# Kernel optimization log

Measured on AMD Instinct MI355X. Metric: run time of the kernel, lower is better.

## Reference

```python
import jax, jax.numpy as jnp
import numpy as np

N = 50000       # nodes
E_RAND = 800000 # random edges (avg degree ~16)
K = 64          # edges touching `node`; setup_inputs guarantees exactly K
F = 64          # num_node_features
C = 64          # conv_channels


def setup_inputs() -> dict:
    key = jax.random.key(0)
    ks = jax.random.split(key, 6)
    x = jax.random.normal(ks[0], (N, F), dtype=jnp.float32)
    # random edges avoiding node 0 so exactly the K prepended edges touch node 0
    src = jax.random.randint(ks[1], (E_RAND,), 1, N, dtype=jnp.int64)
    dst = jax.random.randint(ks[2], (E_RAND,), 1, N, dtype=jnp.int64)
    ksrc = jnp.zeros((K,), dtype=jnp.int64)
    kdst = jnp.arange(1, K + 1, dtype=jnp.int64)
    edge_index = jnp.stack([jnp.concatenate([ksrc, src]),
                            jnp.concatenate([kdst, dst])])  # [2, K+E_RAND]
    W1 = jax.random.normal(ks[3], (F, C), jnp.float32) / np.float32(np.sqrt(F))
    b1 = jnp.zeros((C,), jnp.float32)
    W2 = jax.random.normal(ks[4], (C, C), jnp.float32) / np.float32(np.sqrt(C))
    b2 = jnp.zeros((C,), jnp.float32)
    Wr = jax.random.normal(ks[5], (C, 1), jnp.float32) / np.float32(np.sqrt(C))
    br = jnp.zeros((1,), jnp.float32)
    return {"x": x, "edge_index": edge_index, "node": 0,
            "W1": W1, "b1": b1, "W2": W2, "b2": b2, "Wr": Wr, "br": br}


def gcn_conv(x, src, dst, W, b):
    """PyG GCNConv with self-loops already appended to (src, dst).
    out[v] = sum_{(u,v)} deg(u)^-1/2 * deg(v)^-1/2 * (x @ W)[u] + b
    """
    n = x.shape[0]
    xw = x @ W                                              # [N, C]
    deg = jnp.zeros((n,), xw.dtype).at[dst].add(1.0)        # in-degree incl. self-loop
    dinv = jnp.where(deg > 0, jax.lax.rsqrt(deg), 0.0)
    norm = dinv[src] * dinv[dst]                            # [E]
    out = jax.ops.segment_sum(xw[src] * norm[:, None], dst, num_segments=n)
    return out + b


def reference(x, edge_index, node, W1, b1, W2, b2, Wr, br):
    n = x.shape[0]
    loop = jnp.arange(n, dtype=edge_index.dtype)
    src = jnp.concatenate([edge_index[0], loop])  # add self loops (GCNConv default)
    dst = jnp.concatenate([edge_index[1], loop])
    h = jax.nn.relu(gcn_conv(x, src, dst, W1, b1))
    h = jax.nn.relu(gcn_conv(h, src, dst, W2, b2))
    # edges incident to `node` (setup guarantees exactly K such edges)
    s0, d0 = edge_index[0], edge_index[1]
    mask = (s0 == node) | (d0 == node)
    idx = jnp.nonzero(mask, size=K)[0]
    s, d = s0[idx], d0[idx]
    targets = jnp.where(s == node, d, s)  # self-loop (s==d==node) -> node
    score = h[targets] @ Wr + br          # [K, 1]
    score = jax.nn.softmax(score, axis=0)
    return score[:, 0], targets
```

## Files before the change

kernel.cpp:

```cpp
#include <hip/hip_runtime.h>
#include <math.h>

#define KK 64
#define CAP 64
#define NF 4160
#define BMW 1568

__global__ __launch_bounds__(256) void k_find(const int* __restrict__ ei, int E,
                                              const int* __restrict__ nodep,
                                              int4* __restrict__ zbase, int zcount4,
                                              int* __restrict__ tcount,
                                              int* __restrict__ tpairs,
                                              float* __restrict__ h1s) {
    int idx = blockIdx.x * 256 + threadIdx.x;
    if (idx < zcount4) zbase[idx] = make_int4(0, 0, 0, 0);
    if (idx < 64) h1s[(size_t)NF * 64 + idx] = 0.f;
    int node = nodep[0];
    int n4 = E >> 2;
    if (idx < n4) {
        int4 ss = ((const int4*)ei)[idx];
        int4 dd = ((const int4*)(ei + E))[idx];
        int s[4] = {ss.x, ss.y, ss.z, ss.w};
        int d[4] = {dd.x, dd.y, dd.z, dd.w};
#pragma unroll
        for (int k = 0; k < 4; k++) {
            if (s[k] == node || d[k] == node) {
                int q = atomicAdd(tcount, 1);
                if (q < KK) { int e = idx * 4 + k; tpairs[2 * q] = e; tpairs[2 * q + 1] = (s[k] == node) ? d[k] : s[k]; }
            }
        }
    }
    if (idx == 0) {
        for (int e = n4 * 4; e < E; e++) {
            int s = ei[e], d = ei[E + e];
            if (s == node || d == node) {
                int q = atomicAdd(tcount, 1);
                if (q < KK) { tpairs[2 * q] = e; tpairs[2 * q + 1] = (s == node) ? d : s; }
            }
        }
    }
}

__global__ __launch_bounds__(256) void k_collect_t(const int* __restrict__ ei, int E,
                                                   const int* __restrict__ tpairs,
                                                   int* __restrict__ cnt,
                                                   int* __restrict__ tcnt2,
                                                   int* __restrict__ tslots,
                                                   int* __restrict__ tsorted_g,
                                                   int* __restrict__ towner_g) {
    __shared__ unsigned int bmask[BMW];
    __shared__ int tnode[KK];
    __shared__ int eidx[KK], tgt[KK], srt[KK];
    int tid = threadIdx.x;
    for (int i = tid; i < BMW; i += 256) bmask[i] = 0u;
    if (tid < KK) { eidx[tid] = tpairs[2 * tid]; tgt[tid] = tpairs[2 * tid + 1]; }
    __syncthreads();
    if (tid < KK) {
        int rank = 0;
        for (int j = 0; j < KK; j++) rank += (eidx[j] < eidx[tid]) ? 1 : 0;
        srt[rank] = tgt[tid];
    }
    __syncthreads();
    if (tid < KK) {
        int mynode = srt[tid];
        int owner = tid;
        for (int j = 0; j < tid; j++) if (srt[j] == mynode) { owner = j; break; }
        tnode[tid] = (owner == tid) ? mynode : -1;
        if (owner == tid) atomicOr(&bmask[mynode >> 5], 1u << (mynode & 31));
        if (blockIdx.x == 0) { tsorted_g[tid] = mynode; towner_g[tid] = owner; }
    }
    __syncthreads();
    int n4 = E >> 2;
    for (int idx = blockIdx.x * 256 + tid; idx < n4; idx += gridDim.x * 256) {
        int4 ss = ((const int4*)ei)[idx];
        int4 dd = ((const int4*)(ei + E))[idx];
        int s[4] = {ss.x, ss.y, ss.z, ss.w};
        int d[4] = {dd.x, dd.y, dd.z, dd.w};
        atomicAdd(&cnt[d[0]], 1);
        atomicAdd(&cnt[d[1]], 1);
#pragma unroll
        for (int k = 0; k < 4; k++) {
            if ((bmask[d[k] >> 5] >> (d[k] & 31)) & 1u) {
                int f = 0;
                for (int j = 0; j < KK; j++) if (tnode[j] == d[k]) { f = j + 1; break; }
                if (f) { int p = atomicAdd(&tcnt2[f - 1], 1); if (p < CAP) tslots[(f - 1) * CAP + p] = s[k]; }
            }
        }
    }
    if (blockIdx.x == 0 && tid == 0) {
        for (int e = n4 * 4; e < E; e++) {
            int d = ei[E + e];
            atomicAdd(&cnt[d], 1);
            if ((bmask[d >> 5] >> (d & 31)) & 1u) {
                int f = 0;
                for (int j = 0; j < KK; j++) if (tnode[j] == d) { f = j + 1; break; }
                if (f) { int p = atomicAdd(&tcnt2[f - 1], 1); if (p < CAP) tslots[(f - 1) * CAP + p] = ei[e]; }
            }
        }
    }
}

__device__ __forceinline__ int fnode_of(int i, const int* tsorted, const int* towner,
                                        const int* tcnt2, const int* tslots) {
    int tp = i / 65, j = i % 65;
    if (j == 0) return tsorted[tp];
    int own = towner[tp];
    int c = tcnt2[own]; if (c > CAP) c = CAP;
    return (j - 1 < c) ? tslots[own * CAP + (j - 1)] : -1;
}

__global__ __launch_bounds__(1024) void k_fbuild(const int* __restrict__ tsorted,
                                                 const int* __restrict__ towner,
                                                 const int* __restrict__ tcnt2,
                                                 const int* __restrict__ tslots,
                                                 int* __restrict__ fnode,
                                                 int* __restrict__ fmapRow,
                                                 int* __restrict__ fidx,
                                                 unsigned char* __restrict__ fown) {
    int tid = threadIdx.x;
    for (int i = tid; i < NF; i += 1024)
        fnode[i] = fnode_of(i, tsorted, towner, tcnt2, tslots);
    __syncthreads();
    for (int i = tid; i < NF; i += 1024) {
        int u = fnode[i];
        if (u >= 0) atomicCAS(&fmapRow[u], 0, i + 1);
    }
    __syncthreads();
    for (int i = tid; i < NF; i += 1024) {
        int u = fnode[i];
        if (u >= 0) {
            int row = fmapRow[u];
            fidx[i] = row - 1;
            fown[i] = (unsigned char)(row == i + 1);
        } else {
            fidx[i] = NF;
            fown[i] = 0;
        }
    }
}

__global__ __launch_bounds__(256) void k_collect_f(const int* __restrict__ ei, int E,
                                                   const int* __restrict__ fmapRow,
                                                   int* __restrict__ cnt,
                                                   int* __restrict__ fcnt,
                                                   int* __restrict__ fslots) {
    int idx = blockIdx.x * 256 + threadIdx.x;
    int n4 = E >> 2;
    if (idx < n4) {
        int4 ss = ((const int4*)ei)[idx];
        int4 dd = ((const int4*)(ei + E))[idx];
        int s[4] = {ss.x, ss.y, ss.z, ss.w};
        int d[4] = {dd.x, dd.y, dd.z, dd.w};
        atomicAdd(&cnt[d[2]], 1);
        atomicAdd(&cnt[d[3]], 1);
        int r0 = fmapRow[d[0]], r1 = fmapRow[d[1]], r2 = fmapRow[d[2]], r3 = fmapRow[d[3]];
        if (r0) { int p = atomicAdd(&fcnt[r0 - 1], 1); if (p < CAP) fslots[(size_t)(r0 - 1) * CAP + p] = s[0]; }
        if (r1) { int p = atomicAdd(&fcnt[r1 - 1], 1); if (p < CAP) fslots[(size_t)(r1 - 1) * CAP + p] = s[1]; }
        if (r2) { int p = atomicAdd(&fcnt[r2 - 1], 1); if (p < CAP) fslots[(size_t)(r2 - 1) * CAP + p] = s[2]; }
        if (r3) { int p = atomicAdd(&fcnt[r3 - 1], 1); if (p < CAP) fslots[(size_t)(r3 - 1) * CAP + p] = s[3]; }
    }
    if (idx == 0) {
        for (int e = n4 * 4; e < E; e++) {
            int d = ei[E + e];
            atomicAdd(&cnt[d], 1);
            int r = fmapRow[d];
            if (r) { int p = atomicAdd(&fcnt[r - 1], 1); if (p < CAP) fslots[(size_t)(r - 1) * CAP + p] = ei[e]; }
        }
    }
}

__global__ __launch_bounds__(256) void k_layer1(const float* __restrict__ x,
                                                const int* __restrict__ fnode,
                                                const unsigned char* __restrict__ fown,
                                                const int* __restrict__ cnt,
                                                const int* __restrict__ fcnt,
                                                const int* __restrict__ fslots,
                                                const float* __restrict__ W1,
                                                const float* __restrict__ b1,
                                                float* __restrict__ h1s) {
    __shared__ __align__(16) float W1s[64 * 64];
    __shared__ int anyown;
    int tid = threadIdx.x;
    int i = blockIdx.x * 4 + (tid >> 6);
    int lane = tid & 63;
    int own = (i < NF) ? (int)fown[i] : 0;
    if (tid == 0) anyown = 0;
    __syncthreads();
    if (lane == 0 && own) anyown = 1;
    __syncthreads();
    if (!anyown) return;
    for (int j = tid; j < 1024; j += 256) ((float4*)W1s)[j] = ((const float4*)W1)[j];
    __syncthreads();
    if (!own) return;
    int u = fnode[i];
    float du = rsqrtf((float)(cnt[u] + 1));
    float acc = du * x[(size_t)u * 64 + lane];
    int c = fcnt[i]; if (c > CAP) c = CAP;
    const int* sl = fslots + (size_t)i * CAP;
    int k = 0;
    for (; k + 4 <= c; k += 4) {
        int u0 = sl[k], u1 = sl[k + 1], u2 = sl[k + 2], u3 = sl[k + 3];
        float f0 = rsqrtf((float)(cnt[u0] + 1));
        float f1 = rsqrtf((float)(cnt[u1] + 1));
        float f2 = rsqrtf((float)(cnt[u2] + 1));
        float f3 = rsqrtf((float)(cnt[u3] + 1));
        acc += f0 * x[(size_t)u0 * 64 + lane] + f1 * x[(size_t)u1 * 64 + lane]
             + f2 * x[(size_t)u2 * 64 + lane] + f3 * x[(size_t)u3 * 64 + lane];
    }
    for (; k < c; k++) {
        int uu = sl[k];
        acc += rsqrtf((float)(cnt[uu] + 1)) * x[(size_t)uu * 64 + lane];
    }
    float z = du * acc;
    float h = 0.f;
#pragma unroll
    for (int f = 0; f < 64; f++) h += __shfl(z, f) * W1s[f * 64 + lane];
    h = fmaxf(h + b1[lane], 0.f);
    h1s[(size_t)i * 64 + lane] = du * h;
}

__global__ __launch_bounds__(64) void k_score2(const float* __restrict__ h1s,
                                               const int* __restrict__ fidx,
                                               const int* __restrict__ tsorted,
                                               const int* __restrict__ towner,
                                               const int* __restrict__ tcnt2,
                                               const int* __restrict__ cnt,
                                               const float* __restrict__ W2,
                                               const float* __restrict__ b2,
                                               const float* __restrict__ Wr,
                                               float* __restrict__ sc) {
    int tp = blockIdx.x;
    int lane = threadIdx.x;
    int t = tsorted[tp];
    float dt = rsqrtf((float)(cnt[t] + 1));
    int c = tcnt2[towner[tp]]; if (c > CAP) c = CAP;
    int jmax = 1 + c;
    const int* fx = fidx + tp * 65;
    float z = 0.f;
#pragma unroll 8
    for (int j = 0; j < jmax; j++) {
        int idx = fx[j];
        z += h1s[(size_t)idx * 64 + lane];
    }
    z *= dt;
    float acc = 0.f;
#pragma unroll
    for (int f = 0; f < 64; f++) acc += __shfl(z, f) * W2[f * 64 + lane];
    float h2 = fmaxf(acc + b2[lane], 0.f);
    float p = h2 * Wr[lane];
#pragma unroll
    for (int off = 32; off >= 1; off >>= 1) p += __shfl_xor(p, off);
    if (lane == 0) sc[tp] = p;
}

__global__ void k_softmax(const float* __restrict__ sc, const int* __restrict__ tsorted,
                          float* __restrict__ out) {
    int t = threadIdx.x;
    float s = sc[t];
    float m = s;
#pragma unroll
    for (int off = 32; off >= 1; off >>= 1) m = fmaxf(m, __shfl_xor(m, off));
    float e = __expf(s - m);
    float ss = e;
#pragma unroll
    for (int off = 32; off >= 1; off >>= 1) ss += __shfl_xor(ss, off);
    out[t] = e / ss;
    out[KK + t] = (float)tsorted[t];
}

extern "C" void kernel_launch(void* const* d_in, const int* in_sizes, int n_in,
                              void* d_out, int out_size, void* d_ws, size_t ws_size,
                              hipStream_t stream) {
    const float* x  = (const float*)d_in[0];
    const int*   ei = (const int*)d_in[1];
    const int*   nodep = (const int*)d_in[2];
    const float* W1 = (const float*)d_in[3];
    const float* b1 = (const float*)d_in[4];
    const float* W2 = (const float*)d_in[5];
    const float* b2 = (const float*)d_in[6];
    const float* Wr = (const float*)d_in[7];
    const float* br = (const float*)d_in[8];
    float* out = (float*)d_out;
    (void)br;

    int N = in_sizes[0] / 64;
    int E = in_sizes[1] / 2;

    char* w = (char*)d_ws;
    int* cnt     = (int*)w; w += (size_t)N * 4;
    int* fmapRow = (int*)w; w += (size_t)N * 4;
    int* fcnt    = (int*)w; w += (size_t)NF * 4;
    int* tcnt2   = (int*)w; w += KK * 4;
    int zcount4 = (2 * N + NF + KK) / 4;
    int* tcount = (int*)w; w += 16;
    int* tpairs  = (int*)w; w += 2 * KK * 4;
    int* tsorted = (int*)w; w += KK * 4;
    int* towner  = (int*)w; w += KK * 4;
    int* tslots  = (int*)w; w += (size_t)KK * CAP * 4;
    int* fnode   = (int*)w; w += (size_t)NF * 4;
    int* fidx    = (int*)w; w += (size_t)NF * 4;
    unsigned char* fown = (unsigned char*)w; w += (size_t)NF;
    w = (char*)(((size_t)w + 15) & ~(size_t)15);
    int* fslots  = (int*)w; w += (size_t)NF * CAP * 4;
    float* h1s   = (float*)w; w += (size_t)(NF + 1) * 64 * 4;
    float* sc    = (float*)w; w += KK * 4;

    hipMemsetAsync(tcount, 0, 16, stream);

    int n4 = E >> 2;
    int ebl = (n4 + 255) / 256;
    k_find<<<ebl, 256, 0, stream>>>(ei, E, nodep, (int4*)cnt, zcount4, tcount, tpairs, h1s);
    k_collect_t<<<512, 256, 0, stream>>>(ei, E, tpairs, cnt, tcnt2, tslots, tsorted, towner);
    k_fbuild<<<1, 1024, 0, stream>>>(tsorted, towner, tcnt2, tslots, fnode, fmapRow, fidx, fown);
    k_collect_f<<<ebl, 256, 0, stream>>>(ei, E, fmapRow, cnt, fcnt, fslots);
    k_layer1<<<(NF + 3) / 4, 256, 0, stream>>>(x, fnode, fown, cnt, fcnt, fslots, W1, b1, h1s);
    k_score2<<<KK, 64, 0, stream>>>(h1s, fidx, tsorted, towner, tcnt2, cnt, W2, b2, Wr, sc);
    k_softmax<<<1, 64, 0, stream>>>(sc, tsorted, out);
}
```

Measured before the change: 153.2 us.

## Fold feature-row map construction into collect kernel and drop fbuild launch

Removes the single-block k_fbuild kernel. The node-to-row map (fmapRow) is now built with atomicCAS directly inside k_collect_t, as target and neighbor slots are assigned. k_layer1 and k_score2 derive node ids and ownership on the fly from tslots and fmapRow instead of reading precomputed fnode/fidx/fown arrays. This removes a serialized one-block launch and its global round-trips, at the cost of extra atomics in the edge scan and some indirect lookups in the downstream kernels.

```diff
diff --git a/kernel.cpp b/kernel.cpp
--- a/kernel.cpp
+++ b/kernel.cpp
@@ -10,11 +10,9 @@
                                               const int* __restrict__ nodep,
                                               int4* __restrict__ zbase, int zcount4,
                                               int* __restrict__ tcount,
-                                              int* __restrict__ tpairs,
-                                              float* __restrict__ h1s) {
+                                              int* __restrict__ tpairs) {
     int idx = blockIdx.x * 256 + threadIdx.x;
     if (idx < zcount4) zbase[idx] = make_int4(0, 0, 0, 0);
-    if (idx < 64) h1s[(size_t)NF * 64 + idx] = 0.f;
     int node = nodep[0];
     int n4 = E >> 2;
     if (idx < n4) {
@@ -46,6 +44,7 @@
                                                    int* __restrict__ cnt,
                                                    int* __restrict__ tcnt2,
                                                    int* __restrict__ tslots,
+                                                   int* __restrict__ fmapRow,
                                                    int* __restrict__ tsorted_g,
                                                    int* __restrict__ towner_g) {
     __shared__ unsigned int bmask[BMW];
@@ -67,7 +66,10 @@
         for (int j = 0; j < tid; j++) if (srt[j] == mynode) { owner = j; break; }
         tnode[tid] = (owner == tid) ? mynode : -1;
         if (owner == tid) atomicOr(&bmask[mynode >> 5], 1u << (mynode & 31));
-        if (blockIdx.x == 0) { tsorted_g[tid] = mynode; towner_g[tid] = owner; }
+        if (blockIdx.x == 0) {
+            tsorted_g[tid] = mynode; towner_g[tid] = owner;
+            if (owner == tid) atomicCAS(&fmapRow[mynode], 0, tid * 65 + 0 + 1);
+        }
     }
     __syncthreads();
     int n4 = E >> 2;
@@ -83,7 +85,13 @@
             if ((bmask[d[k] >> 5] >> (d[k] & 31)) & 1u) {
                 int f = 0;
                 for (int j = 0; j < KK; j++) if (tnode[j] == d[k]) { f = j + 1; break; }
-                if (f) { int p = atomicAdd(&tcnt2[f - 1], 1); if (p < CAP) tslots[(f - 1) * CAP + p] = s[k]; }
+                if (f) {
+                    int p = atomicAdd(&tcnt2[f - 1], 1);
+                    if (p < CAP) {
+                        tslots[(f - 1) * CAP + p] = s[k];
+                        atomicCAS(&fmapRow[s[k]], 0, (f - 1) * 65 + (p + 1) + 1);
+                    }
+                }
             }
         }
     }
@@ -94,7 +102,13 @@
             if ((bmask[d >> 5] >> (d & 31)) & 1u) {
                 int f = 0;
                 for (int j = 0; j < KK; j++) if (tnode[j] == d) { f = j + 1; break; }
-                if (f) { int p = atomicAdd(&tcnt2[f - 1], 1); if (p < CAP) tslots[(f - 1) * CAP + p] = ei[e]; }
+                if (f) {
+                    int p = atomicAdd(&tcnt2[f - 1], 1);
+                    if (p < CAP) {
+                        tslots[(f - 1) * CAP + p] = ei[e];
+                        atomicCAS(&fmapRow[ei[e]], 0, (f - 1) * 65 + (p + 1) + 1);
+                    }
+                }
             }
         }
     }
@@ -107,36 +121,6 @@
     int own = towner[tp];
     int c = tcnt2[own]; if (c > CAP) c = CAP;
     return (j - 1 < c) ? tslots[own * CAP + (j - 1)] : -1;
-}
-
-__global__ __launch_bounds__(1024) void k_fbuild(const int* __restrict__ tsorted,
-                                                 const int* __restrict__ towner,
-                                                 const int* __restrict__ tcnt2,
-                                                 const int* __restrict__ tslots,
-                                                 int* __restrict__ fnode,
-                                                 int* __restrict__ fmapRow,
-                                                 int* __restrict__ fidx,
-                                                 unsigned char* __restrict__ fown) {
-    int tid = threadIdx.x;
-    for (int i = tid; i < NF; i += 1024)
-        fnode[i] = fnode_of(i, tsorted, towner, tcnt2, tslots);
-    __syncthreads();
-    for (int i = tid; i < NF; i += 1024) {
-        int u = fnode[i];
-        if (u >= 0) atomicCAS(&fmapRow[u], 0, i + 1);
-    }
-    __syncthreads();
-    for (int i = tid; i < NF; i += 1024) {
-        int u = fnode[i];
-        if (u >= 0) {
-            int row = fmapRow[u];
-            fidx[i] = row - 1;
-            fown[i] = (unsigned char)(row == i + 1);
-        } else {
-            fidx[i] = NF;
-            fown[i] = 0;
-        }
-    }
 }
 
 __global__ __launch_bounds__(256) void k_collect_f(const int* __restrict__ ei, int E,
@@ -161,17 +145,18 @@
     }
     if (idx == 0) {
         for (int e = n4 * 4; e < E; e++) {
-            int d = ei[E + e];
-            atomicAdd(&cnt[d], 1);
-            int r = fmapRow[d];
+            int r = fmapRow[ei[E + e]];
             if (r) { int p = atomicAdd(&fcnt[r - 1], 1); if (p < CAP) fslots[(size_t)(r - 1) * CAP + p] = ei[e]; }
         }
     }
 }
 
 __global__ __launch_bounds__(256) void k_layer1(const float* __restrict__ x,
-                                                const int* __restrict__ fnode,
-                                                const unsigned char* __restrict__ fown,
+                                                const int* __restrict__ tsorted,
+                                                const int* __restrict__ towner,
+                                                const int* __restrict__ tcnt2,
+                                                const int* __restrict__ tslots,
+                                                const int* __restrict__ fmapRow,
                                                 const int* __restrict__ cnt,
                                                 const int* __restrict__ fcnt,
                                                 const int* __restrict__ fslots,
@@ -183,7 +168,11 @@
     int tid = threadIdx.x;
     int i = blockIdx.x * 4 + (tid >> 6);
     int lane = tid & 63;
-    int own = (i < NF) ? (int)fown[i] : 0;
+    int u = -1, own = 0;
+    if (i < NF) {
+        u = fnode_of(i, tsorted, towner, tcnt2, tslots);
+        if (u >= 0) own = (fmapRow[u] == i + 1);
+    }
     if (tid == 0) anyown = 0;
     __syncthreads();
     if (lane == 0 && own) anyown = 1;
@@ -192,7 +181,6 @@
     for (int j = tid; j < 1024; j += 256) ((float4*)W1s)[j] = ((const float4*)W1)[j];
     __syncthreads();
     if (!own) return;
-    int u = fnode[i];
     float du = rsqrtf((float)(cnt[u] + 1));
     float acc = du * x[(size_t)u * 64 + lane];
     int c = fcnt[i]; if (c > CAP) c = CAP;
@@ -220,10 +208,11 @@
 }
 
 __global__ __launch_bounds__(64) void k_score2(const float* __restrict__ h1s,
-                                               const int* __restrict__ fidx,
                                                const int* __restrict__ tsorted,
                                                const int* __restrict__ towner,
                                                const int* __restrict__ tcnt2,
+                                               const int* __restrict__ tslots,
+                                               const int* __restrict__ fmapRow,
                                                const int* __restrict__ cnt,
                                                const float* __restrict__ W2,
                                                const float* __restrict__ b2,
@@ -233,14 +222,15 @@
     int lane = threadIdx.x;
     int t = tsorted[tp];
     float dt = rsqrtf((float)(cnt[t] + 1));
-    int c = tcnt2[towner[tp]]; if (c > CAP) c = CAP;
-    int jmax = 1 + c;
-    const int* fx = fidx + tp * 65;
-    float z = 0.f;
+    int own = towner[tp];
+    int c = tcnt2[own]; if (c > CAP) c = CAP;
+    const int* sl = tslots + own * CAP;
+    float z = h1s[(size_t)(fmapRow[t] - 1) * 64 + lane];
 #pragma unroll 8
-    for (int j = 0; j < jmax; j++) {
-        int idx = fx[j];
-        z += h1s[(size_t)idx * 64 + lane];
+    for (int j = 0; j < c; j++) {
+        int u = sl[j];
+        int row = fmapRow[u] - 1;
+        z += h1s[(size_t)row * 64 + lane];
     }
     z *= dt;
     float acc = 0.f;
@@ -297,23 +287,20 @@
     int* tsorted = (int*)w; w += KK * 4;
     int* towner  = (int*)w; w += KK * 4;
     int* tslots  = (int*)w; w += (size_t)KK * CAP * 4;
-    int* fnode   = (int*)w; w += (size_t)NF * 4;
-    int* fidx    = (int*)w; w += (size_t)NF * 4;
-    unsigned char* fown = (unsigned char*)w; w += (size_t)NF;
-    w = (char*)(((size_t)w + 15) & ~(size_t)15);
     int* fslots  = (int*)w; w += (size_t)NF * CAP * 4;
-    float* h1s   = (float*)w; w += (size_t)(NF + 1) * 64 * 4;
+    float* h1s   = (float*)w; w += (size_t)NF * 64 * 4;
     float* sc    = (float*)w; w += KK * 4;
 
     hipMemsetAsync(tcount, 0, 16, stream);
 
     int n4 = E >> 2;
     int ebl = (n4 + 255) / 256;
-    k_find<<<ebl, 256, 0, stream>>>(ei, E, nodep, (int4*)cnt, zcount4, tcount, tpairs, h1s);
-    k_collect_t<<<512, 256, 0, stream>>>(ei, E, tpairs, cnt, tcnt2, tslots, tsorted, towner);
-    k_fbuild<<<1, 1024, 0, stream>>>(tsorted, towner, tcnt2, tslots, fnode, fmapRow, fidx, fown);
+    k_find<<<ebl, 256, 0, stream>>>(ei, E, nodep, (int4*)cnt, zcount4, tcount, tpairs);
+    k_collect_t<<<512, 256, 0, stream>>>(ei, E, tpairs, cnt, tcnt2, tslots, fmapRow, tsorted, towner);
     k_collect_f<<<ebl, 256, 0, stream>>>(ei, E, fmapRow, cnt, fcnt, fslots);
-    k_layer1<<<(NF + 3) / 4, 256, 0, stream>>>(x, fnode, fown, cnt, fcnt, fslots, W1, b1, h1s);
-    k_score2<<<KK, 64, 0, stream>>>(h1s, fidx, tsorted, towner, tcnt2, cnt, W2, b2, Wr, sc);
+    k_layer1<<<(NF + 3) / 4, 256, 0, stream>>>(x, tsorted, towner, tcnt2, tslots, fmapRow,
+                                               cnt, fcnt, fslots, W1, b1, h1s);
+    k_score2<<<KK, 64, 0, stream>>>(h1s, tsorted, towner, tcnt2, tslots, fmapRow,
+                                    cnt, W2, b2, Wr, sc);
     k_softmax<<<1, 64, 0, stream>>>(sc, tsorted, out);
 }
```

Result: faster. 146.8 us, median of 2 (-4.2%).
